# Optimization experiments

Hardware: AMD Instinct MI355X
Metric: run time of the kernel (lower is better)

## Reference

```python
import jax, jax.numpy as jnp
import numpy as np

SPATIAL_SHAPES = [(128, 128), (64, 64), (32, 32), (16, 16)]  # sum HW = 21760
N_HEADS, N_LEVELS, N_POINTS, EMBED = 8, 4, 4, 256
HEAD_D = EMBED // N_HEADS
B, NQ = 2, 10000
NV = sum(h * w for h, w in SPATIAL_SHAPES)


def setup_inputs() -> dict:
    key = jax.random.key(0)
    ks = jax.random.split(key, 12)
    s = 0.02
    return {
        "query": jax.random.normal(ks[0], (B, NQ, EMBED), jnp.float32),
        "key": jax.random.normal(ks[1], (B, NV, EMBED), jnp.float32),
        "value": jax.random.normal(ks[2], (B, NV, EMBED), jnp.float32),
        "W_off": jax.random.normal(ks[3], (EMBED, N_HEADS * N_LEVELS * N_POINTS * 2), jnp.float32) * s,
        "b_off": jax.random.uniform(ks[4], (N_HEADS * N_LEVELS * N_POINTS * 2,), jnp.float32, -0.9, 0.9),
        "W_attn": jax.random.normal(ks[5], (EMBED, N_HEADS * N_LEVELS * N_POINTS), jnp.float32) * s,
        "b_attn": jnp.zeros((N_HEADS * N_LEVELS * N_POINTS,), jnp.float32),
        "W_v": jax.random.normal(ks[6], (EMBED, EMBED), jnp.float32) * s,
        "b_v": jnp.zeros((EMBED,), jnp.float32),
        "W_out": jax.random.normal(ks[7], (EMBED, EMBED), jnp.float32) * s,
        "b_out": jnp.zeros((EMBED,), jnp.float32),
    }


def bilinear_sample(img, gx, gy):
    """img: [N, Hs, Ws, C]; gx, gy: [N, P] in [-1, 1].
    Torch grid_sample semantics: bilinear, align_corners=True, padding_mode='zeros'.
    gx indexes width, gy indexes height."""
    N, Hs, Ws, C = img.shape
    px = (gx + 1.0) * 0.5 * (Ws - 1)
    py = (gy + 1.0) * 0.5 * (Hs - 1)
    x0 = jnp.floor(px)
    y0 = jnp.floor(py)
    wx = (px - x0)[..., None]
    wy = (py - y0)[..., None]
    x0i = x0.astype(jnp.int32)
    y0i = y0.astype(jnp.int32)
    flat = img.reshape(N, Hs * Ws, C)

    def gather(xi, yi):
        valid = ((xi >= 0) & (xi < Ws) & (yi >= 0) & (yi < Hs))[..., None]
        xc = jnp.clip(xi, 0, Ws - 1)
        yc = jnp.clip(yi, 0, Hs - 1)
        idx = yc * Ws + xc  # [N, P]
        v = jnp.take_along_axis(flat, idx[..., None], axis=1)  # [N, P, C]
        return jnp.where(valid, v, 0.0)

    v00 = gather(x0i, y0i)
    v01 = gather(x0i + 1, y0i)
    v10 = gather(x0i, y0i + 1)
    v11 = gather(x0i + 1, y0i + 1)
    top = v00 * (1.0 - wx) + v01 * wx
    bot = v10 * (1.0 - wx) + v11 * wx
    return top * (1.0 - wy) + bot * wy


def reference(query, key, value, W_off, b_off, W_attn, b_attn, W_v, b_v, W_out, b_out):
    Bq, Nq, _ = query.shape
    # value projection -> per-head values
    v = (value @ W_v + b_v).reshape(Bq, NV, N_HEADS, HEAD_D)
    # sampling locations (used directly as normalized [-1,1] grid coords) and weights
    off = (query @ W_off + b_off).reshape(Bq, Nq, N_HEADS, N_LEVELS, N_POINTS, 2)
    attn = (query @ W_attn + b_attn).reshape(Bq, Nq, N_HEADS, N_LEVELS, N_POINTS)
    attn = jax.nn.softmax(attn, axis=-1)  # softmax over points per level (as in source)

    out = jnp.zeros((Bq, Nq, EMBED), query.dtype)
    start = 0
    for lvl, (Hs, Ws) in enumerate(SPATIAL_SHAPES):
        vl = v[:, start:start + Hs * Ws].reshape(Bq, Hs, Ws, N_HEADS, HEAD_D)
        start += Hs * Ws
        vl = vl.transpose(0, 3, 1, 2, 4).reshape(Bq * N_HEADS, Hs, Ws, HEAD_D)
        gl = off[:, :, :, lvl]  # [B, Nq, H, P, 2]
        gl = gl.transpose(0, 2, 1, 3, 4).reshape(Bq * N_HEADS, Nq * N_POINTS, 2)
        samp = bilinear_sample(vl, gl[..., 0], gl[..., 1])  # [B*H, Nq*P, D]
        samp = samp.reshape(Bq, N_HEADS, Nq, N_POINTS, HEAD_D)
        wl = attn[:, :, :, lvl].transpose(0, 2, 1, 3)  # [B, H, Nq, P]
        out = out + jnp.einsum('bhqp,bhqpd->bqhd', wl, samp).reshape(Bq, Nq, EMBED)
    return out @ W_out + b_out
```

## Files before the change

kernel.cpp:

```cpp
#include <hip/hip_runtime.h>
#include <math.h>

#define B_   2
#define NQ_  10000
#define NV_  21760
#define EMB  256
#define MQ   (B_*NQ_)
#define MV   (B_*NV_)

typedef short bf16x8 __attribute__((ext_vector_type(8)));
typedef float f32x4  __attribute__((ext_vector_type(4)));

__device__ constexpr int LSc[4] = {0, 16384, 20480, 21504};

__device__ __forceinline__ unsigned short f2bf(float x) {
  unsigned u = __builtin_bit_cast(unsigned, x);
  u += 0x7FFFu + ((u >> 16) & 1u);
  return (unsigned short)(u >> 16);
}
__device__ __forceinline__ float bf2f(unsigned short s) {
  return __builtin_bit_cast(float, (unsigned)s << 16);
}

__global__ __launch_bounds__(256) void prep_weights(
    const float* __restrict__ Wv, const float* __restrict__ Wattn,
    const float* __restrict__ Woff, const float* __restrict__ Wout,
    unsigned short* __restrict__ WvT, unsigned short* __restrict__ WoutT,
    unsigned short* __restrict__ WqHi, unsigned short* __restrict__ WqLo) {
  int n = blockIdx.x;
  int k = threadIdx.x;
  if (n < 256) {
    WvT[n * 256 + k] = f2bf(Wv[k * 256 + n]);
  } else if (n < 512) {
    int c = n - 256;
    WoutT[c * 256 + k] = f2bf(Wout[k * 256 + c]);
  } else {
    int qr = n - 512;
    float x = (qr < 256) ? Woff[k * 256 + qr] : Wattn[k * 128 + (qr - 256)];
    unsigned short hi = f2bf(x);
    WqHi[qr * 256 + k] = hi;
    WqLo[qr * 256 + k] = f2bf(x - bf2f(hi));
  }
}

template <int MODE, typename OutT, bool VPERM = false>
__global__ __launch_bounds__(256) void gemm_mfma(
    const void* __restrict__ Aa,
    const unsigned short* __restrict__ Bt, const unsigned short* __restrict__ Bt2,
    const float* __restrict__ bias, const float* __restrict__ bias2,
    OutT* __restrict__ C, unsigned short* __restrict__ C2, int M, int N) {
  constexpr int BM = 128, BK = 32;
  constexpr int SMEM_SHORTS = (MODE == 3 || VPERM) ? 16384 : 8192;
  __shared__ unsigned short smem[SMEM_SHORTS];
  unsigned short* As  = smem;
  unsigned short* Bs  = smem + ((MODE == 3) ? 2 : 1) * BM * BK;
  unsigned short* As2 = smem + BM * BK;
  unsigned short* Bs2 = smem + 3 * BM * BK;

  const int tid = threadIdx.x;
  const int lane = tid & 63, wv = tid >> 6;
  const int wr = wv >> 1, wc = wv & 1;
  const int row0 = blockIdx.x * BM, col0 = blockIdx.y * BM;

  auto lds_addr = [](int row, int kslot) -> int {
    return row * 64 + ((kslot ^ ((row >> 1) & 3)) << 4);
  };

  auto stage_bf = [&](unsigned short* dst, const unsigned short* src,
                      int rbase, int rmax, int kk) {
#pragma unroll
    for (int i = 0; i < 2; ++i) {
      int idx = tid + 256 * i;
      int row = idx >> 2, ks = idx & 3;
      int rg = min(rbase + row, rmax);
      int xorb = (row >> 1) & 3;
      const unsigned short* gp =
          src + (size_t)rg * 256 + kk + ((ks ^ xorb) << 3);
      unsigned short* lp = dst + (size_t)(wv * 64 + i * 256) * 8;
      __builtin_amdgcn_global_load_lds(
          (const __attribute__((address_space(1))) void*)gp,
          (__attribute__((address_space(3))) void*)lp, 16, 0, 0);
    }
  };
  auto stage_cvt = [&](unsigned short* dst, const float* src,
                       int rbase, int rmax, int kk) {
#pragma unroll
    for (int i = 0; i < 4; ++i) {
      int idx = tid + 256 * i;
      int row = idx >> 3, c4 = idx & 7;
      int rg = min(rbase + row, rmax);
      float4 vdat = *(const float4*)(src + (size_t)rg * 256 + kk + c4 * 4);
      ushort4 o;
      o.x = f2bf(vdat.x); o.y = f2bf(vdat.y);
      o.z = f2bf(vdat.z); o.w = f2bf(vdat.w);
      *(ushort4*)((char*)dst + lds_addr(row, c4 >> 1) + (c4 & 1) * 8) = o;
    }
  };
  auto stage_cvt2 = [&](unsigned short* dstH, unsigned short* dstL,
                        const float* src, int rbase, int rmax, int kk) {
#pragma unroll
    for (int i = 0; i < 4; ++i) {
      int idx = tid + 256 * i;
      int row = idx >> 3, c4 = idx & 7;
      int rg = min(rbase + row, rmax);
      float4 vdat = *(const float4*)(src + (size_t)rg * 256 + kk + c4 * 4);
      ushort4 hh, ll;
      hh.x = f2bf(vdat.x); ll.x = f2bf(vdat.x - bf2f(hh.x));
      hh.y = f2bf(vdat.y); ll.y = f2bf(vdat.y - bf2f(hh.y));
      hh.z = f2bf(vdat.z); ll.z = f2bf(vdat.z - bf2f(hh.z));
      hh.w = f2bf(vdat.w); ll.w = f2bf(vdat.w - bf2f(hh.w));
      int a = lds_addr(row, c4 >> 1) + (c4 & 1) * 8;
      *(ushort4*)((char*)dstH + a) = hh;
      *(ushort4*)((char*)dstL + a) = ll;
    }
  };

  const bool three_term = (MODE == 3) && (col0 < 256);

  f32x4 acc[4][4] = {};

  for (int kk = 0; kk < 256; kk += BK) {
    if (kk) __syncthreads();
    if constexpr (MODE == 1)
      stage_cvt(As, (const float*)Aa, row0, M - 1, kk);
    else if constexpr (MODE == 3) {
      if (three_term)
        stage_cvt2(As, As2, (const float*)Aa, row0, M - 1, kk);
      else
        stage_cvt(As, (const float*)Aa, row0, M - 1, kk);
    } else
      stage_bf(As, (const unsigned short*)Aa, row0, M - 1, kk);
    stage_bf(Bs, Bt, col0, N - 1, kk);
    if constexpr (MODE == 3)
      if (three_term) stage_bf(Bs2, Bt2, col0, N - 1, kk);
    __syncthreads();

    const int kslot = lane >> 4;
    bf16x8 af[4], bfr[4];
#pragma unroll
    for (int i = 0; i < 4; ++i) {
      int ra = wr * 64 + i * 16 + (lane & 15);
      af[i] = *(const bf16x8*)((const char*)As + lds_addr(ra, kslot));
      int rb = wc * 64 + i * 16 + (lane & 15);
      bfr[i] = *(const bf16x8*)((const char*)Bs + lds_addr(rb, kslot));
    }
#pragma unroll
    for (int mi = 0; mi < 4; ++mi)
#pragma unroll
      for (int ni = 0; ni < 4; ++ni)
        acc[mi][ni] = __builtin_amdgcn_mfma_f32_16x16x32_bf16(
            af[mi], bfr[ni], acc[mi][ni], 0, 0, 0);

    if constexpr (MODE == 3) {
      if (three_term) {
        bf16x8 af2[4], bfr2[4];
#pragma unroll
        for (int i = 0; i < 4; ++i) {
          int ra = wr * 64 + i * 16 + (lane & 15);
          af2[i] = *(const bf16x8*)((const char*)As2 + lds_addr(ra, kslot));
          int rb = wc * 64 + i * 16 + (lane & 15);
          bfr2[i] = *(const bf16x8*)((const char*)Bs2 + lds_addr(rb, kslot));
        }
#pragma unroll
        for (int mi = 0; mi < 4; ++mi)
#pragma unroll
          for (int ni = 0; ni < 4; ++ni) {
            acc[mi][ni] = __builtin_amdgcn_mfma_f32_16x16x32_bf16(
                af2[mi], bfr[ni], acc[mi][ni], 0, 0, 0);
            acc[mi][ni] = __builtin_amdgcn_mfma_f32_16x16x32_bf16(
                af[mi], bfr2[ni], acc[mi][ni], 0, 0, 0);
          }
      }
    }
  }

  if constexpr (VPERM) {
    float bb4[4];
#pragma unroll
    for (int ni = 0; ni < 4; ++ni)
      bb4[ni] = bias[col0 + wc * 64 + ni * 16 + (lane & 15)];
    __syncthreads();
    unsigned short* pbuf = smem;
#pragma unroll
    for (int mi = 0; mi < 4; ++mi) {
#pragma unroll
      for (int r = 0; r < 4; ++r) {
        int lr = wr * 64 + mi * 16 + ((lane >> 4) << 2) + r;
        int pb = lr >> 1, par = lr & 1;
#pragma unroll
        for (int ni = 0; ni < 4; ++ni) {
          int lc = wc * 64 + ni * 16 + (lane & 15);
          float val = acc[mi][ni][r] + bb4[ni];
          int hl = lc >> 5, d = lc & 31;
          int off = pb * 512 + hl * 128 + ((d >> 2) << 4) + (par << 3) +
                    ((d & 3) << 1);
          *(unsigned short*)((char*)pbuf + off) = f2bf(val);
        }
      }
    }
    __syncthreads();
    int pix0 = row0, bb2 = 0;
    if (pix0 >= NV_) { bb2 = 1; pix0 -= NV_; }
    int lvl = (pix0 >= 16384) + (pix0 >= 20480) + (pix0 >= 21504);
    int rel0 = pix0 - LSc[lvl];
    char* dst = (char*)C + ((size_t)bb2 * NV_ + LSc[lvl]) * 512 +
                (size_t)(rel0 >> 1) * 1024 + (size_t)(col0 >> 5) * 128;
    int pb = tid >> 2, q = tid & 3;
#pragma unroll
    for (int i = 0; i < 8; ++i) {
      int u = q * 16 + i * 64;
      uint4 vd = *(const uint4*)((const char*)pbuf + pb * 512 + u);
      *(uint4*)(dst + (size_t)pb * 1024 + u) = vd;
    }
  } else {
#pragma unroll
    for (int ni = 0; ni < 4; ++ni) {
      int gcol = col0 + wc * 64 + ni * 16 + (lane & 15);
      float bb = (MODE == 3 && gcol >= 256) ? bias2[gcol - 256] : bias[gcol];
#pragma unroll
      for (int mi = 0; mi < 4; ++mi) {
        int rowbase = row0 + wr * 64 + mi * 16 + ((lane >> 4) << 2);
        f32x4 a = acc[mi][ni];
#pragma unroll
        for (int r = 0; r < 4; ++r) {
          int row = rowbase + r;
          if (row < M) {
            float val = a[r] + bb;
            if constexpr (MODE == 3) {
              if (gcol >= 256)
                C2[(size_t)row * 128 + (gcol - 256)] = f2bf(val);
              else
                ((float*)C)[(size_t)row * 256 + gcol] = val;
            } else if constexpr (sizeof(OutT) == 2) {
              C[(size_t)row * N + gcol] = (OutT)f2bf(val);
            } else {
              C[(size_t)row * N + gcol] = (OutT)val;
            }
          }
        }
      }
    }
  }
}

__global__ __launch_bounds__(256) void msda_sample7(
    const char* __restrict__ v,
    const float* __restrict__ off,
    const unsigned short* __restrict__ attnlg,
    ushort4* __restrict__ tmp4) {
  __shared__ unsigned coeff[2 * 136 * 8];
  const int tid = threadIdx.x;
  const int lane = tid & 63;
  const int wid = tid >> 6;
  const int wq = wid >> 1;
  const int w = wid & 1;
  const int bq = blockIdx.x * 2 + wq;
  const int b = (blockIdx.x * 2) / NQ_;

  unsigned* cbase = coeff + wq * (136 * 8);
  const float* offq = off + (size_t)bq * 256;
  const unsigned short* attq = attnlg + (size_t)bq * 128;

  {
    int h = lane >> 3, dl = (lane >> 2) & 1, p = lane & 3;
    int l = 2 * w + dl;
    int Wl = 128 >> l, sh = 7 - l;

    uint2 lg = *(const uint2*)(attq + h * 16 + l * 4);
    float l0 = __builtin_bit_cast(float, lg.x << 16);
    float l1 = __builtin_bit_cast(float, lg.x & 0xFFFF0000u);
    float l2 = __builtin_bit_cast(float, lg.y << 16);
    float l3 = __builtin_bit_cast(float, lg.y & 0xFFFF0000u);
    float m = fmaxf(fmaxf(l0, l1), fmaxf(l2, l3));
    float e0 = expf(l0 - m), e1 = expf(l1 - m);
    float e2 = expf(l2 - m), e3 = expf(l3 - m);
    float ep = (p == 0) ? e0 : (p == 1) ? e1 : (p == 2) ? e2 : e3;
    float wsm = ep / (e0 + e1 + e2 + e3);

    float gx = offq[h * 32 + (l * 4 + p) * 2 + 0];
    float gy = offq[h * 32 + (l * 4 + p) * 2 + 1];
    float s = 0.5f * (float)(Wl - 1);
    float px = fmaf(gx, s, s), py = fmaf(gy, s, s);
    float x0f = floorf(px), y0f = floorf(py);
    float wx = px - x0f, wy = py - y0f;
    int x0 = (int)x0f, y0 = (int)y0f;

    bool bx0 = (unsigned)x0 < (unsigned)Wl, bx1 = (unsigned)(x0 + 1) < (unsigned)Wl;
    bool by0 = (unsigned)y0 < (unsigned)Wl, by1 = (unsigned)(y0 + 1) < (unsigned)Wl;
    int x0c = min(max(x0, 0), Wl - 1), x1c = min(max(x0 + 1, 0), Wl - 1);
    int y0c = min(max(y0, 0), Wl - 1), y1c = min(max(y0 + 1, 0), Wl - 1);

    auto poff = [&](int xx, int yy) -> unsigned {
      return ((unsigned)((yy << (sh - 1)) + (xx >> 1)) << 10) |
             ((unsigned)(xx & 1) << 3);
    };

    float wxm = 1.f - wx, wym = 1.f - wy;
    float w00 = (bx0 & by0) ? wsm * wxm * wym : 0.f;
    float w01 = (bx1 & by0) ? wsm * wx  * wym : 0.f;
    float w10 = (bx0 & by1) ? wsm * wxm * wy  : 0.f;
    float w11 = (bx1 & by1) ? wsm * wx  * wy  : 0.f;

    unsigned* slot = cbase + (h * 17 + l * 4 + p) * 8;
    uint4 s0;
    s0.x = poff(x0c, y0c);
    s0.y = poff(x1c, y0c);
    s0.z = poff(x0c, y1c);
    s0.w = poff(x1c, y1c);
    *(uint4*)slot = s0;
    uint4 s1;
    s1.x = __builtin_bit_cast(unsigned, w00);
    s1.y = __builtin_bit_cast(unsigned, w01);
    s1.z = __builtin_bit_cast(unsigned, w10);
    s1.w = __builtin_bit_cast(unsigned, w11);
    *(uint4*)(slot + 4) = s1;
  }
  __syncthreads();

  const int h = lane >> 3, c4 = lane & 7;
  const unsigned laneoff = (unsigned)(h * 128 + c4 * 16);
  float4 acc = make_float4(0.f, 0.f, 0.f, 0.f);

#pragma unroll
  for (int dl = 0; dl < 2; ++dl) {
    const int l = 2 * w + dl;
    const char* lb = v + ((size_t)b * NV_ + LSc[l]) * 512;
    const unsigned* cb = cbase + (h * 17 + l * 4) * 8;
#pragma unroll
    for (int p = 0; p < 4; ++p) {
      uint4 s0 = *(const uint4*)(cb + p * 8);
      uint4 s1 = *(const uint4*)(cb + p * 8 + 4);
      float w00 = __builtin_bit_cast(float, s1.x);
      float w01 = __builtin_bit_cast(float, s1.y);
      float w10 = __builtin_bit_cast(float, s1.z);
      float w11 = __builtin_bit_cast(float, s1.w);

      uint2 r00 = *(const uint2*)(lb + (laneoff + s0.x));
      uint2 r01 = *(const uint2*)(lb + (laneoff + s0.y));
      uint2 r10 = *(const uint2*)(lb + (laneoff + s0.z));
      uint2 r11 = *(const uint2*)(lb + (laneoff + s0.w));

      acc.x += w00 * __builtin_bit_cast(float, r00.x << 16)
             + w01 * __builtin_bit_cast(float, r01.x << 16)
             + w10 * __builtin_bit_cast(float, r10.x << 16)
             + w11 * __builtin_bit_cast(float, r11.x << 16);
      acc.y += w00 * __builtin_bit_cast(float, r00.x & 0xFFFF0000u)
             + w01 * __builtin_bit_cast(float, r01.x & 0xFFFF0000u)
             + w10 * __builtin_bit_cast(float, r10.x & 0xFFFF0000u)
             + w11 * __builtin_bit_cast(float, r11.x & 0xFFFF0000u);
      acc.z += w00 * __builtin_bit_cast(float, r00.y << 16)
             + w01 * __builtin_bit_cast(float, r01.y << 16)
             + w10 * __builtin_bit_cast(float, r10.y << 16)
             + w11 * __builtin_bit_cast(float, r11.y << 16);
      acc.w += w00 * __builtin_bit_cast(float, r00.y & 0xFFFF0000u)
             + w01 * __builtin_bit_cast(float, r01.y & 0xFFFF0000u)
             + w10 * __builtin_bit_cast(float, r10.y & 0xFFFF0000u)
             + w11 * __builtin_bit_cast(float, r11.y & 0xFFFF0000u);
    }
  }

  __syncthreads();
  float4* red = (float4*)coeff;
  if (w == 1) red[wq * 64 + lane] = acc;
  __syncthreads();
  if (w == 0) {
    float4 o2 = red[wq * 64 + lane];
    acc.x += o2.x; acc.y += o2.y; acc.z += o2.z; acc.w += o2.w;
    ushort4 o;
    o.x = f2bf(acc.x); o.y = f2bf(acc.y); o.z = f2bf(acc.z); o.w = f2bf(acc.w);
    tmp4[(size_t)bq * 64 + lane] = o;
  }
}

extern "C" void kernel_launch(void* const* d_in, const int* in_sizes, int n_in,
                              void* d_out, int out_size, void* d_ws, size_t ws_size,
                              hipStream_t stream) {
  const float* query  = (const float*)d_in[0];
  const float* value  = (const float*)d_in[2];
  const float* W_off  = (const float*)d_in[3];
  const float* b_off  = (const float*)d_in[4];
  const float* W_attn = (const float*)d_in[5];
  const float* b_attn = (const float*)d_in[6];
  const float* W_v    = (const float*)d_in[7];
  const float* b_v    = (const float*)d_in[8];
  const float* W_out  = (const float*)d_in[9];
  const float* b_out  = (const float*)d_in[10];
  float* out = (float*)d_out;

  char* p = (char*)d_ws;
  unsigned short* v_bf  = (unsigned short*)p; p += (size_t)MV * 256 * 2;
  float*          off_w = (float*)p;          p += (size_t)MQ * 256 * 4;
  unsigned short* att_w = (unsigned short*)p; p += (size_t)MQ * 128 * 2;
  unsigned short* tmp_bf= (unsigned short*)p; p += (size_t)MQ * 256 * 2;
  unsigned short* WvT   = (unsigned short*)p; p += 256 * 256 * 2;
  unsigned short* WoutT = (unsigned short*)p; p += 256 * 256 * 2;
  unsigned short* WqHi  = (unsigned short*)p; p += 384 * 256 * 2;
  unsigned short* WqLo  = (unsigned short*)p; p += 384 * 256 * 2;

  prep_weights<<<dim3(896), dim3(256), 0, stream>>>(
      W_v, W_attn, W_off, W_out, WvT, WoutT, WqHi, WqLo);

  gemm_mfma<1, unsigned short, true><<<dim3(MV / 128, 2), dim3(256), 0, stream>>>(
      value, WvT, nullptr, b_v, nullptr, v_bf, nullptr, MV, 256);

  gemm_mfma<3, float><<<dim3((MQ + 127) / 128, 3), dim3(256), 0, stream>>>(
      query, WqHi, WqLo, b_off, b_attn, off_w, att_w, MQ, 384);

  msda_sample7<<<dim3(MQ / 2), dim3(256), 0, stream>>>(
      (const char*)v_bf, off_w, att_w, (ushort4*)tmp_bf);

  gemm_mfma<0, float><<<dim3((MQ + 127) / 128, 2), dim3(256), 0, stream>>>(
      tmp_bf, WoutT, nullptr, b_out, nullptr, out, nullptr, MQ, 256);
}
```

Baseline: 120.2 us.

## Tile weight transpose through shared memory and rebalance level pairs across waves

The weight prep kernel now transposes 32-column tiles through padded shared memory, so global reads are coalesced, instead of doing strided per-element reads across 896 blocks; it now launches 28 blocks. In the sampling kernel each wave pair now handles levels {0,3} and {1,2} instead of {0,1} and {2,3}. This spreads the large level-0 and small level-3 maps across waves to balance cache footprint and memory traffic. The tradeoff is that the new prep kernel writes each row serially through 32 scalar stores per thread and uses very few blocks.

```diff
diff --git a/kernel.cpp b/kernel.cpp
--- a/kernel.cpp
+++ b/kernel.cpp
@@ -27,19 +27,40 @@
     const float* __restrict__ Woff, const float* __restrict__ Wout,
     unsigned short* __restrict__ WvT, unsigned short* __restrict__ WoutT,
     unsigned short* __restrict__ WqHi, unsigned short* __restrict__ WqLo) {
-  int n = blockIdx.x;
-  int k = threadIdx.x;
-  if (n < 256) {
-    WvT[n * 256 + k] = f2bf(Wv[k * 256 + n]);
-  } else if (n < 512) {
-    int c = n - 256;
-    WoutT[c * 256 + k] = f2bf(Wout[k * 256 + c]);
-  } else {
-    int qr = n - 512;
-    float x = (qr < 256) ? Woff[k * 256 + qr] : Wattn[k * 128 + (qr - 256)];
+  __shared__ float tile[32][257];
+  const int bid = blockIdx.x;
+  const float* src;
+  int n0, which, ncols;
+  if (bid < 8)       { which = 0; src = Wv;    n0 = bid * 32;        ncols = 256; }
+  else if (bid < 16) { which = 1; src = Wout;  n0 = (bid - 8) * 32;  ncols = 256; }
+  else if (bid < 24) { which = 2; src = Woff;  n0 = (bid - 16) * 32; ncols = 256; }
+  else               { which = 3; src = Wattn; n0 = (bid - 24) * 32; ncols = 128; }
+
+  const int tc = threadIdx.x & 31;
+  const int tk = threadIdx.x >> 5;
+#pragma unroll
+  for (int i = 0; i < 32; ++i) {
+    int k = tk + 8 * i;
+    tile[tc][k] = src[(size_t)k * ncols + n0 + tc];
+  }
+  __syncthreads();
+
+  const int n = threadIdx.x >> 3;
+  const int kc = (threadIdx.x & 7) * 32;
+  unsigned short* dh;
+  unsigned short* dl = nullptr;
+  if (which == 0)      dh = WvT   + (size_t)(n0 + n) * 256;
+  else if (which == 1) dh = WoutT + (size_t)(n0 + n) * 256;
+  else if (which == 2) { dh = WqHi + (size_t)(n0 + n) * 256;
+                         dl = WqLo + (size_t)(n0 + n) * 256; }
+  else                 { dh = WqHi + (size_t)(256 + n0 + n) * 256;
+                         dl = WqLo + (size_t)(256 + n0 + n) * 256; }
+#pragma unroll
+  for (int j = 0; j < 32; ++j) {
+    float x = tile[n][kc + j];
     unsigned short hi = f2bf(x);
-    WqHi[qr * 256 + k] = hi;
-    WqLo[qr * 256 + k] = f2bf(x - bf2f(hi));
+    dh[kc + j] = hi;
+    if (dl) dl[kc + j] = f2bf(x - bf2f(hi));
   }
 }
 
@@ -263,7 +284,7 @@
 
   {
     int h = lane >> 3, dl = (lane >> 2) & 1, p = lane & 3;
-    int l = 2 * w + dl;
+    int l = dl ? (3 - w) : w;
     int Wl = 128 >> l, sh = 7 - l;
 
     uint2 lg = *(const uint2*)(attq + h * 16 + l * 4);
@@ -323,7 +344,7 @@
 
 #pragma unroll
   for (int dl = 0; dl < 2; ++dl) {
-    const int l = 2 * w + dl;
+    const int l = dl ? (3 - w) : w;
     const char* lb = v + ((size_t)b * NV_ + LSc[l]) * 512;
     const unsigned* cb = cbase + (h * 17 + l * 4) * 8;
 #pragma unroll
@@ -397,7 +418,7 @@
   unsigned short* WqHi  = (unsigned short*)p; p += 384 * 256 * 2;
   unsigned short* WqLo  = (unsigned short*)p; p += 384 * 256 * 2;
 
-  prep_weights<<<dim3(896), dim3(256), 0, stream>>>(
+  prep_weights<<<dim3(28), dim3(256), 0, stream>>>(
       W_v, W_attn, W_off, W_out, WvT, WoutT, WqHi, WqLo);
 
   gemm_mfma<1, unsigned short, true><<<dim3(MV / 128, 2), dim3(256), 0, stream>>>(
```

Result: slower. 125.2 us (+4.1%).
